# Kernel optimization log

Hardware: AMD Instinct MI355X
Metric: run time of the kernel (lower is better)

The kernel has to match this reference:

```python
import jax, jax.numpy as jnp
import numpy as np

EPS = 1e-3       # sinkhorn eps (init kwarg)
MAX_ITER = 100   # init kwarg

B, N, H, W = 16, 1024, 32, 32

def setup_inputs() -> dict:
    key = jax.random.key(0)
    k1, k2 = jax.random.split(key)
    x = jax.random.normal(k1, (B, N, H, W), dtype=jnp.float32)
    y = jax.random.normal(k2, (B, N, H, W), dtype=jnp.float32)
    return {"x": x, "y": y}

def _l2_normalize(a, axis=-1, eps=1e-12):
    # matches F.normalize(p=2): divide by max(norm, eps)
    n = jnp.sqrt(jnp.sum(a * a, axis=axis, keepdims=True))
    return a / jnp.maximum(n, eps)

def reference(x, y):
    b, n = x.shape[0], x.shape[1]
    xf = _l2_normalize(x.reshape(b, n, -1))          # [B,N,D], unit rows
    yf = _l2_normalize(y.reshape(b, n, -1))
    # cosine similarity of unit vectors == dot product -> GEMM instead of
    # the O(N^2 D) broadcasted intermediate in the torch source (same math)
    cost = 1.0 - jnp.einsum('bnd,bmd->bnm', xf, yf)  # [B,N,N]
    cost = cost / jnp.max(cost)                      # global max, as in torch .max()

    u0 = jnp.full((b, n), 1.0 / n, dtype=cost.dtype)
    v0 = jnp.full((b, n), 1.0 / n, dtype=cost.dtype)

    def step(carry, _):
        u, v = carry
        u = 1.0 / (jnp.einsum('bnm,bm->bn', cost, v) + EPS)
        v = 1.0 / (jnp.einsum('bnm,bn->bm', cost, u) + EPS)
        return (u, v), None

    (u, v), _ = jax.lax.scan(step, (u0, v0), None, length=MAX_ITER)

    # sum over both point dims of u_i * C_ij * v_j, then mean over batch
    distance = jnp.einsum('bn,bnm,bm->b', u, cost, v)
    return jnp.mean(distance)
```

## Files before the change

### kernel.cpp

```cpp
#include <hip/hip_runtime.h>

#define NBATCH 16
#define NPTS   1024
#define NDIM   1024
#define EPSI   1e-3f
#define QSCALE 127.5f
#define SPIN_TIMEOUT_TICKS (1ull << 28)

typedef __attribute__((ext_vector_type(8))) short short8;
typedef __attribute__((ext_vector_type(4))) float f32x4;
typedef __attribute__((ext_vector_type(4))) unsigned uint32x4;

__device__ __forceinline__ unsigned short f2bf(float f) {
  union { float f; unsigned u; } v; v.f = f;
  unsigned r = v.u + 0x7fffu + ((v.u >> 16) & 1u);
  return (unsigned short)(r >> 16);
}

__device__ __forceinline__ void st_agent(float* p, float v) {
  __hip_atomic_store(p, v, __ATOMIC_RELAXED, __HIP_MEMORY_SCOPE_AGENT);
}
__device__ __forceinline__ unsigned long long ld_agent64(const unsigned long long* p) {
  return __hip_atomic_load(p, __ATOMIC_RELAXED, __HIP_MEMORY_SCOPE_AGENT);
}

__global__ __launch_bounds__(256) void norm_kernel(const float* __restrict__ x,
                                                   const float* __restrict__ y,
                                                   unsigned short* __restrict__ xf,
                                                   unsigned short* __restrict__ yf) {
  int row = blockIdx.x;
  const float* src; unsigned short* dst;
  if (row < NBATCH * NPTS) { src = x; dst = xf; }
  else { row -= NBATCH * NPTS; src = y; dst = yf; }
  src += (size_t)row * NDIM; dst += (size_t)row * NDIM;
  const int t = threadIdx.x;
  float4 val = ((const float4*)src)[t];
  float ss = val.x*val.x + val.y*val.y + val.z*val.z + val.w*val.w;
  #pragma unroll
  for (int o = 32; o; o >>= 1) ss += __shfl_xor(ss, o, 64);
  __shared__ float wsum[4];
  if ((t & 63) == 0) wsum[t >> 6] = ss;
  __syncthreads();
  float tot = wsum[0] + wsum[1] + wsum[2] + wsum[3];
  float inv = 1.0f / fmaxf(sqrtf(tot), 1e-12f);
  ushort4 o4;
  o4.x = f2bf(val.x * inv); o4.y = f2bf(val.y * inv);
  o4.z = f2bf(val.z * inv); o4.w = f2bf(val.w * inv);
  ((ushort4*)dst)[t] = o4;
}

#define GLD_LDS16(g, l) __builtin_amdgcn_global_load_lds( \
    (const __attribute__((address_space(1))) unsigned int*)(g), \
    (__attribute__((address_space(3))) unsigned int*)(l), 16, 0, 0)

__device__ __forceinline__ unsigned char q8(float cv) {
  float t = cv * QSCALE + 0.5f;
  t = fminf(fmaxf(t, 0.f), 255.f);
  return (unsigned char)(int)t;
}

__global__ __launch_bounds__(256) void gemm_cost(const unsigned short* __restrict__ A,
                                                 const unsigned short* __restrict__ B,
                                                 unsigned char* __restrict__ Cq,
                                                 unsigned char* __restrict__ CTq,
                                                 unsigned* __restrict__ cmax_bits) {
  const int b = blockIdx.z;
  const int bm = blockIdx.y * 128, bn = blockIdx.x * 128;
  const int t = threadIdx.x, lane = t & 63, wv = t >> 6;
  const int wm = (wv & 1) * 64, wn = (wv >> 1) * 64;
  __shared__ unsigned short As[128 * 32];
  __shared__ unsigned short Bs[128 * 32];
  f32x4 acc[4][4];
  #pragma unroll
  for (int i = 0; i < 4; ++i)
    #pragma unroll
    for (int j = 0; j < 4; ++j) acc[i][j] = (f32x4){0.f, 0.f, 0.f, 0.f};

  const unsigned short* gA = A + (size_t)b*NPTS*NDIM + (size_t)(bm + (t >> 2))*NDIM + (t & 3)*8;
  const unsigned short* gB = B + (size_t)b*NPTS*NDIM + (size_t)(bn + (t >> 2))*NDIM + (t & 3)*8;
  const int ar = lane & 15, ak = (lane >> 4) * 8;

  for (int k0 = 0; k0 < NDIM; k0 += 32) {
    GLD_LDS16(gA + k0,             As + t*8);
    GLD_LDS16(gA + 64*NDIM + k0,   As + 2048 + t*8);
    GLD_LDS16(gB + k0,             Bs + t*8);
    GLD_LDS16(gB + 64*NDIM + k0,   Bs + 2048 + t*8);
    __syncthreads();
    short8 af[4], bq[4];
    #pragma unroll
    for (int i = 0; i < 4; ++i) af[i] = *(const short8*)(As + (wm + i*16 + ar)*32 + ak);
    #pragma unroll
    for (int j = 0; j < 4; ++j) bq[j] = *(const short8*)(Bs + (wn + j*16 + ar)*32 + ak);
    #pragma unroll
    for (int i = 0; i < 4; ++i)
      #pragma unroll
      for (int j = 0; j < 4; ++j)
        acc[i][j] = __builtin_amdgcn_mfma_f32_16x16x32_bf16(af[i], bq[j], acc[i][j], 0, 0, 0);
    __syncthreads();
  }

  float mx = 0.f;
  const int cr = (lane >> 4) * 4, cc = lane & 15;
  unsigned char* Cb = Cq  + (size_t)b * NPTS * NPTS;
  unsigned char* Tb = CTq + (size_t)b * NPTS * NPTS;
  #pragma unroll
  for (int i = 0; i < 4; ++i) {
    #pragma unroll
    for (int j = 0; j < 4; ++j) {
      const int row0 = bm + wm + i*16 + cr;
      const int col  = bn + wn + j*16 + cc;
      #pragma unroll
      for (int r = 0; r < 4; ++r) {
        float cv = 1.0f - acc[i][j][r];
        mx = fmaxf(mx, cv);
        unsigned char qv = q8(cv);
        Cb[(size_t)(row0 + r) * NPTS + col] = qv;
        Tb[(size_t)col * NPTS + row0 + r]   = qv;
      }
    }
  }
  #pragma unroll
  for (int o = 32; o; o >>= 1) mx = fmaxf(mx, __shfl_xor(mx, o, 64));
  if (lane == 0) atomicMax(cmax_bits, __float_as_uint(mx));
}


__device__ __forceinline__ float dot16(uint32x4 q, f32x4 g0, f32x4 g1, f32x4 g2, f32x4 g3) {
  float a = 0.f;
  a += (float)( q.x        & 0xffu) * g0.x;
  a += (float)((q.x >>  8) & 0xffu) * g0.y;
  a += (float)((q.x >> 16) & 0xffu) * g0.z;
  a += (float)( q.x >> 24         ) * g0.w;
  a += (float)( q.y        & 0xffu) * g1.x;
  a += (float)((q.y >>  8) & 0xffu) * g1.y;
  a += (float)((q.y >> 16) & 0xffu) * g1.z;
  a += (float)( q.y >> 24         ) * g1.w;
  a += (float)( q.z        & 0xffu) * g2.x;
  a += (float)((q.z >>  8) & 0xffu) * g2.y;
  a += (float)((q.z >> 16) & 0xffu) * g2.z;
  a += (float)( q.z >> 24         ) * g2.w;
  a += (float)( q.w        & 0xffu) * g3.x;
  a += (float)((q.w >>  8) & 0xffu) * g3.y;
  a += (float)((q.w >> 16) & 0xffu) * g3.z;
  a += (float)( q.w >> 24         ) * g3.w;
  return a;
}

#define LOAD_G(buf)                                          \
  const f32x4 g0 = *(const f32x4*)&buf[      lane * 4];      \
  const f32x4 g1 = *(const f32x4*)&buf[256 + lane * 4];      \
  const f32x4 g2 = *(const f32x4*)&buf[512 + lane * 4];      \
  const f32x4 g3 = *(const f32x4*)&buf[768 + lane * 4];

__global__ __launch_bounds__(512) void sinkhorn_kernel(
    const unsigned char* __restrict__ Cq, const unsigned char* __restrict__ CTq,
    float* __restrict__ part, unsigned* __restrict__ bar, float* __restrict__ dist,
    const unsigned* __restrict__ cmax_bits)
{
  const int wg = blockIdx.x;
  const int b = wg & (NBATCH - 1);
  const int s = wg >> 4;
  const int ob = s * 64;
  const int tid = threadIdx.x, lane = tid & 63, w = tid >> 6;

  __shared__ __align__(16) float gst[1024];
  __shared__ __align__(16) float lds_u[64];
  __shared__ float dred[8];
  __shared__ int s_tmo;
  if (tid == 0) s_tmo = 0;

  const float cmax  = __uint_as_float(*cmax_bits);
  const float invc2 = 1.0f / (QSCALE * cmax);

  uint32x4 mc[8];
  {
    const unsigned char* cb = Cq + (size_t)b * NPTS * NPTS;
    #pragma unroll
    for (int p = 0; p < 8; ++p)
      mc[p] = *(const uint32x4*)(cb + (size_t)(ob + w * 8 + p) * NPTS + lane * 16);
  }
  uint32x4 md0[4], md1[4];
  {
    const unsigned char* tb = CTq + (size_t)b * NPTS * NPTS;
    const int c0 = w * 128 + lane;
    #pragma unroll
    for (int j = 0; j < 4; ++j) {
      md0[j] = *(const uint32x4*)(tb + (size_t)c0 * NPTS + ob + j * 16);
      md1[j] = *(const uint32x4*)(tb + (size_t)(c0 + 64) * NPTS + ob + j * 16);
    }
  }

  unsigned* barb = bar + b * 64;

  gst[tid]       = 1.0f / (float)NPTS;
  gst[tid + 512] = 1.0f / (float)NPTS;
  const int i0 = ((tid >> 1) & 3) * 256 + (tid >> 3) * 4 + (tid & 1) * 2;
  __syncthreads();

  unsigned bt = 16;
  #pragma unroll 1
  for (int it = 0; it < 100; ++it) {
    LOAD_G(gst);
    float myu = 0.f;
    #pragma unroll
    for (int p = 0; p < 8; ++p) {
      float acc = dot16(mc[p], g0, g1, g2, g3);
      #pragma unroll
      for (int o = 32; o; o >>= 1) acc += __shfl_xor(acc, o, 64);
      const float val = 1.0f / (acc * invc2 + EPSI);
      myu = (lane == p) ? val : myu;
    }
    if (lane < 8) lds_u[w * 8 + lane] = myu;
    __syncthreads();

    float p0 = 0.f, p1 = 0.f;
    #pragma unroll
    for (int q = 0; q < 16; ++q) {
      const float4 uq = *(const float4*)&lds_u[4 * q];
      const unsigned d0 = md0[q >> 2][q & 3];
      const unsigned d1 = md1[q >> 2][q & 3];
      p0 += (float)( d0        & 0xffu) * uq.x;
      p0 += (float)((d0 >>  8) & 0xffu) * uq.y;
      p0 += (float)((d0 >> 16) & 0xffu) * uq.z;
      p0 += (float)( d0 >> 24         ) * uq.w;
      p1 += (float)( d1        & 0xffu) * uq.x;
      p1 += (float)((d1 >>  8) & 0xffu) * uq.y;
      p1 += (float)((d1 >> 16) & 0xffu) * uq.z;
      p1 += (float)( d1 >> 24         ) * uq.w;
    }
    float* pw = part + ((size_t)((it & 1) * NBATCH + b) * 16 + s) * 1024 + w * 128;
    st_agent(pw + lane,      p0);
    st_agent(pw + 64 + lane, p1);

    __syncthreads();
    if (tid == 0) {
      __hip_atomic_fetch_add(barb, 1u, __ATOMIC_RELEASE, __HIP_MEMORY_SCOPE_AGENT);
      if (!s_tmo) {
        int polls = 0; unsigned long long t0 = 0;
        while (__hip_atomic_load(barb, __ATOMIC_RELAXED, __HIP_MEMORY_SCOPE_AGENT) < bt) {
          __builtin_amdgcn_s_sleep(1);
          if ((++polls & 63) == 0) {
            if (!t0) t0 = __builtin_amdgcn_s_memrealtime();
            else if (__builtin_amdgcn_s_memrealtime() - t0 > SPIN_TIMEOUT_TICKS) { s_tmo = 1; break; }
          }
        }
      }
      asm volatile("" ::: "memory");
    }
    __syncthreads();
    bt += 16;

    const float* prb = part + (size_t)((it & 1) * NBATCH + b) * 16 * 1024;
    float r0 = 0.f, r1 = 0.f;
    #pragma unroll
    for (int q = 0; q < 16; ++q) {
      union { unsigned long long u; float f[2]; } c;
      c.u = ld_agent64((const unsigned long long*)(prb + q * 1024) + tid);
      r0 += c.f[0]; r1 += c.f[1];
    }
    const float v0 = 1.0f / (r0 * invc2 + EPSI);
    const float v1 = 1.0f / (r1 * invc2 + EPSI);
    gst[i0]     = v0;
    gst[i0 + 1] = v1;

    if (it == 99 && s == 0) {
      float dterm = v0 * r0 + v1 * r1;
      #pragma unroll
      for (int o = 32; o; o >>= 1) dterm += __shfl_xor(dterm, o, 64);
      if (lane == 0) dred[w] = dterm;
    }
    __syncthreads();
  }

  if (s == 0 && tid == 0) {
    float d = 0.f;
    #pragma unroll
    for (int ww = 0; ww < 8; ++ww) d += dred[ww];
    st_agent(&dist[b], d * invc2);
  }
}

__global__ void finalize_kernel(const float* __restrict__ dist, float* __restrict__ out) {
  if (threadIdx.x == 0) {
    float s = 0.f;
    for (int i = 0; i < NBATCH; ++i) s += dist[i];
    out[0] = s * (1.0f / NBATCH);
  }
}

extern "C" void kernel_launch(void* const* d_in, const int* in_sizes, int n_in,
                              void* d_out, int out_size, void* d_ws, size_t ws_size,
                              hipStream_t stream) {
  (void)in_sizes; (void)n_in; (void)out_size; (void)ws_size;
  const float* x = (const float*)d_in[0];
  const float* y = (const float*)d_in[1];
  float* out = (float*)d_out;
  char* ws = (char*)d_ws;

  unsigned* cmax_bits = (unsigned*)ws;
  unsigned* bar       = (unsigned*)(ws + 4096);
  float*    dist      = (float*)(ws + 8192);
  const size_t MB = 1u << 20;
  float*    part      = (float*)(ws + 2*MB);
  unsigned short* xf = (unsigned short*)(ws + 1*MB);
  unsigned short* yf = (unsigned short*)(ws + 33*MB);
  unsigned char*  C  = (unsigned char*)(ws + 65*MB);
  unsigned char*  CT = (unsigned char*)(ws + 81*MB);

  hipMemsetAsync(d_ws, 0, 65536, stream);

  hipLaunchKernelGGL(norm_kernel, dim3(2 * NBATCH * NPTS), dim3(256), 0, stream, x, y, xf, yf);
  hipLaunchKernelGGL(gemm_cost, dim3(8, 8, NBATCH), dim3(256), 0, stream, xf, yf, C, CT, cmax_bits);
  hipLaunchKernelGGL(sinkhorn_kernel, dim3(256), dim3(512), 0, stream, C, CT, part, bar, dist, cmax_bits);
  hipLaunchKernelGGL(finalize_kernel, dim3(1), dim3(64), 0, stream, dist, out);
}
```

Measured before the change: 1.226 ms.

## Replace all-gather reduction with reduce-scatter plus all-gather of v

Each workgroup previously read all 16 partial slices of the full 1024-entry vector after one grid barrier, then computed v redundantly. Now each workgroup reduces only its own 64-entry slice, writes v to a shared buffer, and a second barrier lets all workgroups gather the full v. This cuts per-iteration global reads from 16 KB to about 4 KB per workgroup, but adds a second cross-workgroup barrier per iteration. The distance term is now accumulated per slice and scaled in the finalize kernel.

```diff
diff --git a/kernel.cpp b/kernel.cpp
--- a/kernel.cpp
+++ b/kernel.cpp
@@ -17,6 +17,9 @@
   return (unsigned short)(r >> 16);
 }
 
+__device__ __forceinline__ float ld_agent(const float* p) {
+  return __hip_atomic_load(p, __ATOMIC_RELAXED, __HIP_MEMORY_SCOPE_AGENT);
+}
 __device__ __forceinline__ void st_agent(float* p, float v) {
   __hip_atomic_store(p, v, __ATOMIC_RELAXED, __HIP_MEMORY_SCOPE_AGENT);
 }
@@ -152,10 +155,29 @@
   const f32x4 g2 = *(const f32x4*)&buf[512 + lane * 4];      \
   const f32x4 g3 = *(const f32x4*)&buf[768 + lane * 4];
 
+__device__ __forceinline__ void bar_sync(unsigned* barb, unsigned target, int* s_tmo,
+                                         int tid) {
+  if (tid == 0) {
+    __hip_atomic_fetch_add(barb, 1u, __ATOMIC_RELEASE, __HIP_MEMORY_SCOPE_AGENT);
+    if (!*s_tmo) {
+      int polls = 0; unsigned long long t0 = 0;
+      while (__hip_atomic_load(barb, __ATOMIC_RELAXED, __HIP_MEMORY_SCOPE_AGENT) < target) {
+        __builtin_amdgcn_s_sleep(1);
+        if ((++polls & 63) == 0) {
+          if (!t0) t0 = __builtin_amdgcn_s_memrealtime();
+          else if (__builtin_amdgcn_s_memrealtime() - t0 > SPIN_TIMEOUT_TICKS) { *s_tmo = 1; break; }
+        }
+      }
+    }
+    asm volatile("" ::: "memory");
+  }
+  __syncthreads();
+}
+
 __global__ __launch_bounds__(512) void sinkhorn_kernel(
     const unsigned char* __restrict__ Cq, const unsigned char* __restrict__ CTq,
-    float* __restrict__ part, unsigned* __restrict__ bar, float* __restrict__ dist,
-    const unsigned* __restrict__ cmax_bits)
+    float* __restrict__ part, float* __restrict__ vbuf, unsigned* __restrict__ bar,
+    float* __restrict__ dslice, const unsigned* __restrict__ cmax_bits)
 {
   const int wg = blockIdx.x;
   const int b = wg & (NBATCH - 1);
@@ -165,7 +187,7 @@
 
   __shared__ __align__(16) float gst[1024];
   __shared__ __align__(16) float lds_u[64];
-  __shared__ float dred[8];
+  __shared__ float red[8][64];
   __shared__ int s_tmo;
   if (tid == 0) s_tmo = 0;
 
@@ -191,6 +213,7 @@
   }
 
   unsigned* barb = bar + b * 64;
+  float* vb = vbuf + b * NPTS;
 
   gst[tid]       = 1.0f / (float)NPTS;
   gst[tid + 512] = 1.0f / (float)NPTS;
@@ -228,63 +251,53 @@
       p1 += (float)((d1 >> 16) & 0xffu) * uq.z;
       p1 += (float)( d1 >> 24         ) * uq.w;
     }
-    float* pw = part + ((size_t)((it & 1) * NBATCH + b) * 16 + s) * 1024 + w * 128;
-    st_agent(pw + lane,      p0);
-    st_agent(pw + 64 + lane, p1);
-
-    __syncthreads();
-    if (tid == 0) {
-      __hip_atomic_fetch_add(barb, 1u, __ATOMIC_RELEASE, __HIP_MEMORY_SCOPE_AGENT);
-      if (!s_tmo) {
-        int polls = 0; unsigned long long t0 = 0;
-        while (__hip_atomic_load(barb, __ATOMIC_RELAXED, __HIP_MEMORY_SCOPE_AGENT) < bt) {
-          __builtin_amdgcn_s_sleep(1);
-          if ((++polls & 63) == 0) {
-            if (!t0) t0 = __builtin_amdgcn_s_memrealtime();
-            else if (__builtin_amdgcn_s_memrealtime() - t0 > SPIN_TIMEOUT_TICKS) { s_tmo = 1; break; }
-          }
-        }
+    float* pb = part + (size_t)((it & 1) * NBATCH + b) * (16 * 16 * 64);
+    st_agent(pb + ((2 * w    ) * 16 + s) * 64 + lane, p0);
+    st_agent(pb + ((2 * w + 1) * 16 + s) * 64 + lane, p1);
+
+    __syncthreads();
+    bar_sync(barb, bt, &s_tmo, tid); bt += 16;
+
+    {
+      const float* blk = pb + s * (16 * 64);
+      const float q0 = ld_agent(blk + (2 * w    ) * 64 + lane);
+      const float q1 = ld_agent(blk + (2 * w + 1) * 64 + lane);
+      red[w][lane] = q0 + q1;
+    }
+    __syncthreads();
+    if (tid < 64) {
+      float raw = red[0][tid];
+      #pragma unroll
+      for (int ww = 1; ww < 8; ++ww) raw += red[ww][tid];
+      const float vm = 1.0f / (raw * invc2 + EPSI);
+      st_agent(&vb[ob + tid], vm);
+      if (it == 99) {
+        float dterm = vm * raw;
+        #pragma unroll
+        for (int o = 32; o; o >>= 1) dterm += __shfl_xor(dterm, o, 64);
+        if (tid == 0) st_agent(&dslice[b * 16 + s], dterm);
       }
-      asm volatile("" ::: "memory");
-    }
-    __syncthreads();
-    bt += 16;
-
-    const float* prb = part + (size_t)((it & 1) * NBATCH + b) * 16 * 1024;
-    float r0 = 0.f, r1 = 0.f;
-    #pragma unroll
-    for (int q = 0; q < 16; ++q) {
+    }
+
+    __syncthreads();
+    bar_sync(barb, bt, &s_tmo, tid); bt += 16;
+    {
       union { unsigned long long u; float f[2]; } c;
-      c.u = ld_agent64((const unsigned long long*)(prb + q * 1024) + tid);
-      r0 += c.f[0]; r1 += c.f[1];
-    }
-    const float v0 = 1.0f / (r0 * invc2 + EPSI);
-    const float v1 = 1.0f / (r1 * invc2 + EPSI);
-    gst[i0]     = v0;
-    gst[i0 + 1] = v1;
-
-    if (it == 99 && s == 0) {
-      float dterm = v0 * r0 + v1 * r1;
-      #pragma unroll
-      for (int o = 32; o; o >>= 1) dterm += __shfl_xor(dterm, o, 64);
-      if (lane == 0) dred[w] = dterm;
-    }
-    __syncthreads();
-  }
-
-  if (s == 0 && tid == 0) {
-    float d = 0.f;
-    #pragma unroll
-    for (int ww = 0; ww < 8; ++ww) d += dred[ww];
-    st_agent(&dist[b], d * invc2);
-  }
-}
-
-__global__ void finalize_kernel(const float* __restrict__ dist, float* __restrict__ out) {
+      c.u = ld_agent64((const unsigned long long*)vb + tid);
+      gst[i0]     = c.f[0];
+      gst[i0 + 1] = c.f[1];
+    }
+    __syncthreads();
+  }
+}
+
+__global__ void finalize_kernel(const float* __restrict__ dslice, float* __restrict__ out,
+                                const unsigned* __restrict__ cmax_bits) {
   if (threadIdx.x == 0) {
+    const float invc2 = 1.0f / (QSCALE * __uint_as_float(*cmax_bits));
     float s = 0.f;
-    for (int i = 0; i < NBATCH; ++i) s += dist[i];
-    out[0] = s * (1.0f / NBATCH);
+    for (int i = 0; i < NBATCH * 16; ++i) s += dslice[i];
+    out[0] = s * invc2 * (1.0f / NBATCH);
   }
 }
 
@@ -299,7 +312,8 @@
 
   unsigned* cmax_bits = (unsigned*)ws;
   unsigned* bar       = (unsigned*)(ws + 4096);
-  float*    dist      = (float*)(ws + 8192);
+  float*    dslice    = (float*)(ws + 8192);
+  float*    vbuf      = (float*)(ws + 65536);
   const size_t MB = 1u << 20;
   float*    part      = (float*)(ws + 2*MB);
   unsigned short* xf = (unsigned short*)(ws + 1*MB);
@@ -311,6 +325,6 @@
 
   hipLaunchKernelGGL(norm_kernel, dim3(2 * NBATCH * NPTS), dim3(256), 0, stream, x, y, xf, yf);
   hipLaunchKernelGGL(gemm_cost, dim3(8, 8, NBATCH), dim3(256), 0, stream, xf, yf, C, CT, cmax_bits);
-  hipLaunchKernelGGL(sinkhorn_kernel, dim3(256), dim3(512), 0, stream, C, CT, part, bar, dist, cmax_bits);
-  hipLaunchKernelGGL(finalize_kernel, dim3(1), dim3(64), 0, stream, dist, out);
-}
+  hipLaunchKernelGGL(sinkhorn_kernel, dim3(256), dim3(512), 0, stream, C, CT, part, vbuf, bar, dslice, cmax_bits);
+  hipLaunchKernelGGL(finalize_kernel, dim3(1), dim3(64), 0, stream, dslice, out, cmax_bits);
+}
```

After: 1.768 ms. 1.44x slower.
